# Performance work log

Hardware: AMD Instinct MI355X
Metric: run time of the kernel (lower is better)

## Reference

```python
import jax, jax.numpy as jnp
import numpy as np

EPS = 1e-10


def setup_inputs() -> dict:
    key = jax.random.key(0)
    k1, k2 = jax.random.split(key)
    inputs = jax.random.normal(k1, (32, 64, 64, 64), dtype=jnp.float32)
    # tf.random_uniform_initializer() default: U(-0.05, 0.05)
    embeddings = jax.random.uniform(k2, (1024, 64), dtype=jnp.float32,
                                    minval=-0.05, maxval=0.05)
    return {"inputs": inputs, "embeddings": embeddings}


def reference(inputs, embeddings):
    beta = 0.25
    K, D = embeddings.shape
    input_shape = inputs.shape
    flat = inputs.reshape(-1, D)                      # [N, D]

    # squared L2 distances: |a|^2 - 2 a.b + |b|^2  -> [N, K]
    a_sq = jnp.sum(flat * flat, axis=1, keepdims=True)
    ab = 2.0 * (flat @ embeddings.T)
    b_sq = jnp.sum(embeddings * embeddings, axis=1)[None, :]
    distances = a_sq - ab + b_sq

    idx = jnp.argmin(distances, axis=1)               # [N]
    # gather nearest codes (equivalent to one_hot @ embeddings)
    quantized = embeddings[idx].reshape(input_shape)

    commitment_loss = jnp.mean(jnp.square(jax.lax.stop_gradient(quantized) - inputs))
    codebook_loss = jnp.mean(jnp.square(quantized - jax.lax.stop_gradient(inputs)))
    vq_loss = commitment_loss + beta * codebook_loss

    # straight-through estimator
    quantized_st = inputs + jax.lax.stop_gradient(quantized - inputs)

    # perplexity from code usage histogram (== mean of one-hot rows)
    N = flat.shape[0]
    counts = jnp.zeros((K,), dtype=jnp.float32).at[idx].add(1.0)
    avg_probs = counts / N
    perplexity = jnp.exp(-jnp.sum(avg_probs * jnp.log(avg_probs + EPS)))

    indices_reshaped = idx.reshape(input_shape[:-1])
    return quantized_st, indices_reshaped, perplexity, vq_loss
```

## Files before the change

kernel.cpp:

```cpp
#include <hip/hip_runtime.h>
#include <float.h>

#define N_ROWS 131072
#define DIM 64
#define KCODES 1024
#define TAU_HALF 5.0e-4f
#define FLAGBIT 0x200000
#define NBLOCKA (N_ROWS / 128)
#define NPART (NBLOCKA * 4)
#define NBLOCKF (N_ROWS * 4 / 256)

typedef __attribute__((ext_vector_type(8))) short short8;
typedef __attribute__((ext_vector_type(4))) float f32x4;

__device__ __forceinline__ unsigned short f2bf_rne(float x) {
    unsigned int u = __float_as_uint(x);
    unsigned int r = u + 0x7FFFu + ((u >> 16) & 1u);
    return (unsigned short)(r >> 16);
}
__device__ __forceinline__ float bf2f(unsigned short h) {
    return __uint_as_float(((unsigned int)h) << 16);
}

__device__ __forceinline__ float np_pairwise_sq64(const float* v) {
    float r[8];
#pragma unroll
    for (int j = 0; j < 8; ++j) r[j] = __fmul_rn(v[j], v[j]);
#pragma unroll
    for (int i = 8; i < 64; i += 8)
#pragma unroll
        for (int j = 0; j < 8; ++j)
            r[j] = __fadd_rn(r[j], __fmul_rn(v[i + j], v[i + j]));
    return __fadd_rn(
        __fadd_rn(__fadd_rn(r[0], r[1]), __fadd_rn(r[2], r[3])),
        __fadd_rn(__fadd_rn(r[4], r[5]), __fadd_rn(r[6], r[7])));
}

__device__ __forceinline__ float np_sq_stream(const float* xr) {
    float r[8];
    {
        float4 a = *reinterpret_cast<const float4*>(xr);
        float4 b = *reinterpret_cast<const float4*>(xr + 4);
        r[0] = __fmul_rn(a.x, a.x); r[1] = __fmul_rn(a.y, a.y);
        r[2] = __fmul_rn(a.z, a.z); r[3] = __fmul_rn(a.w, a.w);
        r[4] = __fmul_rn(b.x, b.x); r[5] = __fmul_rn(b.y, b.y);
        r[6] = __fmul_rn(b.z, b.z); r[7] = __fmul_rn(b.w, b.w);
    }
#pragma unroll
    for (int i = 8; i < 64; i += 8) {
        float4 a = *reinterpret_cast<const float4*>(xr + i);
        float4 b = *reinterpret_cast<const float4*>(xr + i + 4);
        r[0] = __fadd_rn(r[0], __fmul_rn(a.x, a.x));
        r[1] = __fadd_rn(r[1], __fmul_rn(a.y, a.y));
        r[2] = __fadd_rn(r[2], __fmul_rn(a.z, a.z));
        r[3] = __fadd_rn(r[3], __fmul_rn(a.w, a.w));
        r[4] = __fadd_rn(r[4], __fmul_rn(b.x, b.x));
        r[5] = __fadd_rn(r[5], __fmul_rn(b.y, b.y));
        r[6] = __fadd_rn(r[6], __fmul_rn(b.z, b.z));
        r[7] = __fadd_rn(r[7], __fmul_rn(b.w, b.w));
    }
    return __fadd_rn(
        __fadd_rn(__fadd_rn(r[0], r[1]), __fadd_rn(r[2], r[3])),
        __fadd_rn(__fadd_rn(r[4], r[5]), __fadd_rn(r[6], r[7])));
}

__device__ __forceinline__ float np_dist_stream(const float* xr, const float* e,
                                                float a_sq, float bq) {
    double acc0 = 0.0, acc1 = 0.0, acc2 = 0.0, acc3 = 0.0;
#pragma unroll
    for (int d = 0; d < DIM; d += 4) {
        float4 ev = *reinterpret_cast<const float4*>(e + d);
        float4 xv = *reinterpret_cast<const float4*>(xr + d);
        acc0 = fma((double)xv.x, (double)ev.x, acc0);
        acc1 = fma((double)xv.y, (double)ev.y, acc1);
        acc2 = fma((double)xv.z, (double)ev.z, acc2);
        acc3 = fma((double)xv.w, (double)ev.w, acc3);
    }
    double dot = (acc0 + acc1) + (acc2 + acc3);
    float ab = (float)(2.0 * dot);
    return __fadd_rn(__fsub_rn(a_sq, ab), bq);
}

__global__ __launch_bounds__(256, 4)
void vq_prep(const float* __restrict__ emb,
             int* __restrict__ hist,
             float* __restrict__ bsqf,
             unsigned short* __restrict__ epack) {
    const int tid = blockIdx.x * 256 + threadIdx.x;
    const int c   = tid >> 4;
    const int sub = tid & 15;
    const int g   = sub & 7;
    const int lvl = sub >> 3;

    const float* e8 = emb + (size_t)c * DIM + g * 8;
    float4 v0 = *reinterpret_cast<const float4*>(e8);
    float4 v1 = *reinterpret_cast<const float4*>(e8 + 4);
    float ev[8] = {v0.x, v0.y, v0.z, v0.w, v1.x, v1.y, v1.z, v1.w};
    short8 outv;
#pragma unroll
    for (int j = 0; j < 8; ++j) {
        unsigned short hh = f2bf_rne(ev[j]);
        outv[j] = (lvl == 0) ? (short)hh : (short)f2bf_rne(ev[j] - bf2f(hh));
    }
    const size_t base =
        ((((size_t)(c >> 4) * 2 + lvl) * 2 + (g >> 2)) * 64 +
         (((g & 3) << 4) | (c & 15))) * 8;
    *reinterpret_cast<short8*>(epack + base) = outv;

    if (sub == 0) {
        float e[DIM];
        const float4* src = reinterpret_cast<const float4*>(emb + (size_t)c * DIM);
#pragma unroll
        for (int i = 0; i < DIM / 4; ++i) {
            float4 v = src[i];
            e[i * 4 + 0] = v.x; e[i * 4 + 1] = v.y;
            e[i * 4 + 2] = v.z; e[i * 4 + 3] = v.w;
        }
        bsqf[c] = np_pairwise_sq64(e);
        hist[c] = 0;
    }
}

__global__ __launch_bounds__(256, 4)
void vq_fast(const float* __restrict__ x,
             const unsigned short* __restrict__ epack,
             const float* __restrict__ bsqf,
             float* __restrict__ idxout,
             float* __restrict__ partials) {
    __shared__ unsigned short lds[16384];
    __shared__ float bql[KCODES];
    __shared__ float aql[4][2][16];

    const int t = threadIdx.x;
    const int lane = t & 63;
    const int wid = t >> 6;
    const int rowbase = blockIdx.x * 128 + wid * 32;
    const int arow = lane & 15;
    const int kgrp = lane >> 4;

#pragma unroll
    for (int i = 0; i < 4; ++i) bql[t + i * 256] = bsqf[t + i * 256];

    short8 ah[2][2], al[2][2];
#pragma unroll
    for (int mf = 0; mf < 2; ++mf) {
        float ssq = 0.f;
#pragma unroll
        for (int kt = 0; kt < 2; ++kt) {
            const float* src = x + (size_t)(rowbase + mf * 16 + arow) * DIM + kt * 32 + kgrp * 8;
            float4 v0 = *reinterpret_cast<const float4*>(src);
            float4 v1 = *reinterpret_cast<const float4*>(src + 4);
            float xv[8] = {v0.x, v0.y, v0.z, v0.w, v1.x, v1.y, v1.z, v1.w};
            short8 h, l;
#pragma unroll
            for (int j = 0; j < 8; ++j) {
                unsigned short hh = f2bf_rne(xv[j]);
                h[j] = (short)hh;
                l[j] = (short)f2bf_rne(xv[j] - bf2f(hh));
                ssq = fmaf(xv[j], xv[j], ssq);
            }
            ah[mf][kt] = h;
            al[mf][kt] = l;
        }
        ssq += __shfl_xor(ssq, 16);
        ssq += __shfl_xor(ssq, 32);
        if (kgrp == 0) aql[wid][mf][arow] = ssq;
    }

    float best[2][4], sec[2][4];
    int bidx[2][4], sidx[2][4];
#pragma unroll
    for (int mf = 0; mf < 2; ++mf)
#pragma unroll
        for (int r = 0; r < 4; ++r) {
            best[mf][r] = -FLT_MAX; sec[mf][r] = -FLT_MAX;
            bidx[mf][r] = 0; sidx[mf][r] = 0;
        }

    for (int ch = 0; ch < 8; ++ch) {
        __syncthreads();
        {
            const float4* gsrc = reinterpret_cast<const float4*>(epack + (size_t)ch * 16384);
            float4* ldst = reinterpret_cast<float4*>(lds);
#pragma unroll
            for (int i = 0; i < 8; ++i)
                ldst[t + i * 256] = gsrc[t + i * 256];
        }
        __syncthreads();

        for (int ctl = 0; ctl < 8; ++ctl) {
            const int code0 = (ch * 8 + ctl) * 16;
            const unsigned short* fb = lds + ctl * 2048 + lane * 8;
            short8 bh0 = *reinterpret_cast<const short8*>(fb + 0 * 512);
            short8 bh1 = *reinterpret_cast<const short8*>(fb + 1 * 512);
            short8 bl0 = *reinterpret_cast<const short8*>(fb + 2 * 512);
            short8 bl1 = *reinterpret_cast<const short8*>(fb + 3 * 512);
            const float nb = -0.5f * bql[code0 + arow];

            f32x4 acc[2];
#pragma unroll
            for (int mf = 0; mf < 2; ++mf) {
                f32x4 a = {nb, nb, nb, nb};
                a = __builtin_amdgcn_mfma_f32_16x16x32_bf16(ah[mf][0], bh0, a, 0, 0, 0);
                a = __builtin_amdgcn_mfma_f32_16x16x32_bf16(ah[mf][1], bh1, a, 0, 0, 0);
                a = __builtin_amdgcn_mfma_f32_16x16x32_bf16(ah[mf][0], bl0, a, 0, 0, 0);
                a = __builtin_amdgcn_mfma_f32_16x16x32_bf16(ah[mf][1], bl1, a, 0, 0, 0);
                a = __builtin_amdgcn_mfma_f32_16x16x32_bf16(al[mf][0], bh0, a, 0, 0, 0);
                a = __builtin_amdgcn_mfma_f32_16x16x32_bf16(al[mf][1], bh1, a, 0, 0, 0);
                acc[mf] = a;
            }

            const int code = code0 + arow;
#pragma unroll
            for (int mf = 0; mf < 2; ++mf)
#pragma unroll
                for (int r = 0; r < 4; ++r) {
                    float m = acc[mf][r];
                    bool gt_b = m > best[mf][r];
                    bool gt_s = m > sec[mf][r];
                    sec[mf][r]  = gt_b ? best[mf][r] : (gt_s ? m : sec[mf][r]);
                    sidx[mf][r] = gt_b ? bidx[mf][r] : (gt_s ? code : sidx[mf][r]);
                    best[mf][r] = gt_b ? m : best[mf][r];
                    bidx[mf][r] = gt_b ? code : bidx[mf][r];
                }
        }
    }

#pragma unroll
    for (int mf = 0; mf < 2; ++mf)
#pragma unroll
        for (int r = 0; r < 4; ++r) {
            float b = best[mf][r], sc = sec[mf][r];
            int bi = bidx[mf][r], si = sidx[mf][r];
#pragma unroll
            for (int off = 1; off < 16; off <<= 1) {
                float ob  = __shfl_xor(b, off);
                int   obi = __shfl_xor(bi, off);
                float osc = __shfl_xor(sc, off);
                int   osi = __shfl_xor(si, off);
                bool o_gt = ob > b;
                float loser  = o_gt ? b  : ob;
                int   loseri = o_gt ? bi : obi;
                b  = o_gt ? ob  : b;
                bi = o_gt ? obi : bi;
                float ns = sc; int nsi = si;
                if (osc > ns)   { ns = osc;   nsi = osi; }
                if (loser > ns) { ns = loser; nsi = loseri; }
                sc = ns; si = nsi;
            }
            best[mf][r] = b; sec[mf][r] = sc;
            bidx[mf][r] = bi; sidx[mf][r] = si;
        }

    if ((lane & 15) == 0) {
        const int rgrp = lane >> 4;
        float lsum = 0.f;
#pragma unroll
        for (int mf = 0; mf < 2; ++mf)
#pragma unroll
            for (int r = 0; r < 4; ++r) {
                int rl = rgrp * 4 + r;
                int row = rowbase + mf * 16 + rl;
                int bi = bidx[mf][r], si = sidx[mf][r];
                int lo = min(bi, si), hi = max(bi, si);
                bool flag = (best[mf][r] - sec[mf][r]) <= TAU_HALF;
                int enc = flag ? (FLAGBIT | lo | (hi << 10)) : bi;
                idxout[row] = (float)enc;
                lsum += fmaf(-2.0f, best[mf][r], aql[wid][mf][rl]);
            }
        lsum += __shfl_xor(lsum, 16);
        lsum += __shfl_xor(lsum, 32);
        if (lane == 0) partials[blockIdx.x * 4 + wid] = lsum;
    }
}

__global__ __launch_bounds__(256, 8)
void vq_finalize(const float* __restrict__ x,
                 const float* __restrict__ emb,
                 const float* __restrict__ bsqf,
                 float* __restrict__ idxout,
                 float* __restrict__ qout,
                 int* __restrict__ hist) {
    const int gid  = blockIdx.x * 256 + threadIdx.x;
    const int row  = gid >> 2;
    const int part = gid & 3;
    int v = (int)idxout[row];
    int k;
    if (v & FLAGBIT) {
        const int c1 = v & 1023;
        const int c2 = (v >> 10) & 1023;
        const float* xr = x + (size_t)row * DIM;
        float a_sq = np_sq_stream(xr);
        float d1 = np_dist_stream(xr, emb + (size_t)c1 * DIM, a_sq, bsqf[c1]);
        float d2 = np_dist_stream(xr, emb + (size_t)c2 * DIM, a_sq, bsqf[c2]);
        k = (d2 < d1) ? c2 : c1;
        if (part == 0) idxout[row] = (float)k;
    } else {
        k = v;
    }

    const float4* er = reinterpret_cast<const float4*>(emb + (size_t)k * DIM + part * 16);
    float4* qr = reinterpret_cast<float4*>(qout + (size_t)row * DIM + part * 16);
#pragma unroll
    for (int i = 0; i < 4; ++i) qr[i] = er[i];
    if (part == 0) atomicAdd(&hist[k], 1);
}

__global__ void vq_final(const int* __restrict__ hist,
                         const float* __restrict__ partials,
                         float* __restrict__ out2) {
    __shared__ double sh[KCODES];
    __shared__ double sl[KCODES];
    int t = threadIdx.x;

    double p = (double)hist[t] * (1.0 / (double)N_ROWS);
    sh[t] = p * log(p + 1e-10);

    double ls = 0.0;
#pragma unroll
    for (int i = 0; i < NPART / KCODES; ++i)
        ls += (double)partials[t + i * KCODES];
    sl[t] = ls;
    __syncthreads();

    for (int off = KCODES / 2; off > 0; off >>= 1) {
        if (t < off) { sh[t] += sh[t + off]; sl[t] += sl[t + off]; }
        __syncthreads();
    }
    if (t == 0) {
        out2[0] = (float)exp(-sh[0]);
        out2[1] = (float)(1.25 * sl[0] * (1.0 / (double)((size_t)N_ROWS * DIM)));
    }
}

extern "C" void kernel_launch(void* const* d_in, const int* in_sizes, int n_in,
                              void* d_out, int out_size, void* d_ws, size_t ws_size,
                              hipStream_t stream) {
    const float* x   = (const float*)d_in[0];
    const float* emb = (const float*)d_in[1];
    float* out = (float*)d_out;

    int*   hist      = (int*)d_ws;
    float* bsqf      = (float*)((char*)d_ws + 4096);
    float* partials  = (float*)((char*)d_ws + 8192);
    unsigned short* epack = (unsigned short*)((char*)d_ws + 40960);

    float* qout    = out;
    float* idxout  = out + 8388608;
    float* scalars = out + 8388608 + 131072;

    vq_prep    <<<64, 256, 0, stream>>>(emb, hist, bsqf, epack);
    vq_fast    <<<NBLOCKA, 256, 0, stream>>>(x, epack, bsqf, idxout, partials);
    vq_finalize<<<NBLOCKF, 256, 0, stream>>>(x, emb, bsqf, idxout, qout, hist);
    vq_final   <<<1, KCODES, 0, stream>>>(hist, partials, scalars);
}
```

Measured before the change: 123.8 us.

## Fuse near-tie refinement and quantized gather into the main VQ kernel

Removes the separate finalize kernel. The main kernel now resolves flagged near-tie rows in place with exact fp32 distances, stores the chosen indices in shared memory, and has the whole block write the quantized rows, indices and histogram atomics. This drops one launch and the write-then-reread of the encoded index buffer. In exchange the refinement runs serially on one lane per 16, which can diverge and lengthen the tail of the main kernel, and the fused kernel now carries more registers and extra barriers.

New measurement: 110.8 us. 1.12x faster.

```diff
diff --git a/kernel.cpp b/kernel.cpp
--- a/kernel.cpp
+++ b/kernel.cpp
@@ -5,10 +5,8 @@
 #define DIM 64
 #define KCODES 1024
 #define TAU_HALF 5.0e-4f
-#define FLAGBIT 0x200000
 #define NBLOCKA (N_ROWS / 128)
 #define NPART (NBLOCKA * 4)
-#define NBLOCKF (N_ROWS * 4 / 256)
 
 typedef __attribute__((ext_vector_type(8))) short short8;
 typedef __attribute__((ext_vector_type(4))) float f32x4;
@@ -123,9 +121,12 @@
 
 __global__ __launch_bounds__(256, 4)
 void vq_fast(const float* __restrict__ x,
+             const float* __restrict__ emb,
              const unsigned short* __restrict__ epack,
              const float* __restrict__ bsqf,
              float* __restrict__ idxout,
+             float* __restrict__ qout,
+             int* __restrict__ hist,
              float* __restrict__ partials) {
     __shared__ unsigned short lds[16384];
     __shared__ float bql[KCODES];
@@ -252,6 +253,9 @@
             bidx[mf][r] = bi; sidx[mf][r] = si;
         }
 
+    __syncthreads();
+    int* ldsK = reinterpret_cast<int*>(lds);
+
     if ((lane & 15) == 0) {
         const int rgrp = lane >> 4;
         float lsum = 0.f;
@@ -260,50 +264,42 @@
 #pragma unroll
             for (int r = 0; r < 4; ++r) {
                 int rl = rgrp * 4 + r;
-                int row = rowbase + mf * 16 + rl;
+                int rloc = wid * 32 + mf * 16 + rl;
                 int bi = bidx[mf][r], si = sidx[mf][r];
-                int lo = min(bi, si), hi = max(bi, si);
-                bool flag = (best[mf][r] - sec[mf][r]) <= TAU_HALF;
-                int enc = flag ? (FLAGBIT | lo | (hi << 10)) : bi;
-                idxout[row] = (float)enc;
+                int k = bi;
+                if (best[mf][r] - sec[mf][r] <= TAU_HALF) {
+                    int c1 = min(bi, si), c2 = max(bi, si);
+                    const float* xr = x + (size_t)(rowbase - wid * 32 + rloc) * DIM;
+                    float a_sq = np_sq_stream(xr);
+                    float d1 = np_dist_stream(xr, emb + (size_t)c1 * DIM, a_sq, bql[c1]);
+                    float d2 = np_dist_stream(xr, emb + (size_t)c2 * DIM, a_sq, bql[c2]);
+                    k = (d2 < d1) ? c2 : c1;
+                }
+                ldsK[rloc] = k;
                 lsum += fmaf(-2.0f, best[mf][r], aql[wid][mf][rl]);
             }
         lsum += __shfl_xor(lsum, 16);
         lsum += __shfl_xor(lsum, 32);
         if (lane == 0) partials[blockIdx.x * 4 + wid] = lsum;
     }
-}
-
-__global__ __launch_bounds__(256, 8)
-void vq_finalize(const float* __restrict__ x,
-                 const float* __restrict__ emb,
-                 const float* __restrict__ bsqf,
-                 float* __restrict__ idxout,
-                 float* __restrict__ qout,
-                 int* __restrict__ hist) {
-    const int gid  = blockIdx.x * 256 + threadIdx.x;
-    const int row  = gid >> 2;
-    const int part = gid & 3;
-    int v = (int)idxout[row];
-    int k;
-    if (v & FLAGBIT) {
-        const int c1 = v & 1023;
-        const int c2 = (v >> 10) & 1023;
-        const float* xr = x + (size_t)row * DIM;
-        float a_sq = np_sq_stream(xr);
-        float d1 = np_dist_stream(xr, emb + (size_t)c1 * DIM, a_sq, bsqf[c1]);
-        float d2 = np_dist_stream(xr, emb + (size_t)c2 * DIM, a_sq, bsqf[c2]);
-        k = (d2 < d1) ? c2 : c1;
-        if (part == 0) idxout[row] = (float)k;
-    } else {
-        k = v;
-    }
-
-    const float4* er = reinterpret_cast<const float4*>(emb + (size_t)k * DIM + part * 16);
-    float4* qr = reinterpret_cast<float4*>(qout + (size_t)row * DIM + part * 16);
-#pragma unroll
-    for (int i = 0; i < 4; ++i) qr[i] = er[i];
-    if (part == 0) atomicAdd(&hist[k], 1);
+    __syncthreads();
+
+    const int blkrow0 = blockIdx.x * 128;
+#pragma unroll
+    for (int s = 0; s < 2; ++s) {
+        int slice = t + s * 256;
+        int rl    = slice >> 2;
+        int part  = slice & 3;
+        int k     = ldsK[rl];
+        int row   = blkrow0 + rl;
+        const float4* er = reinterpret_cast<const float4*>(emb + (size_t)k * DIM + part * 16);
+        float4* qr = reinterpret_cast<float4*>(qout + (size_t)row * DIM + part * 16);
+        qr[0] = er[0]; qr[1] = er[1]; qr[2] = er[2]; qr[3] = er[3];
+        if (part == 0) {
+            idxout[row] = (float)k;
+            atomicAdd(&hist[k], 1);
+        }
+    }
 }
 
 __global__ void vq_final(const int* __restrict__ hist,
@@ -349,8 +345,8 @@
     float* idxout  = out + 8388608;
     float* scalars = out + 8388608 + 131072;
 
-    vq_prep    <<<64, 256, 0, stream>>>(emb, hist, bsqf, epack);
-    vq_fast    <<<NBLOCKA, 256, 0, stream>>>(x, epack, bsqf, idxout, partials);
-    vq_finalize<<<NBLOCKF, 256, 0, stream>>>(x, emb, bsqf, idxout, qout, hist);
-    vq_final   <<<1, KCODES, 0, stream>>>(hist, partials, scalars);
-}
+    vq_prep <<<64, 256, 0, stream>>>(emb, hist, bsqf, epack);
+    vq_fast <<<NBLOCKA, 256, 0, stream>>>(x, emb, epack, bsqf, idxout, qout,
+                                          hist, partials);
+    vq_final<<<1, KCODES, 0, stream>>>(hist, partials, scalars);
+}
```
